# Performance work log

Hardware: AMD Instinct MI355X
Metric: run time of the kernel (lower is better)

## Reference

```python
import jax, jax.numpy as jnp
import numpy as np

NL, ND, NM = 16384, 4096, 2048   # LncRNA / Disease / MiRNA node counts
E = 262144                       # edges per relation
FEAT, HID, OUTF = 256, 64, 128
ITEMS, SIZE = 4096, 2048


def setup_inputs() -> dict:
    key = jax.random.key(0)
    ks = jax.random.split(key, 32)
    f32 = jnp.float32

    def ed(i, n_src, n_dst):
        return (jax.random.randint(ks[i], (E,), 0, n_src),
                jax.random.randint(ks[i + 1], (E,), 0, n_dst))

    src_LD, dst_LD = ed(0, NL, ND)
    src_DL, dst_DL = ed(2, ND, NL)
    src_LM, dst_LM = ed(4, NL, NM)
    src_ML, dst_ML = ed(6, NM, NL)
    src_DM, dst_DM = ed(8, ND, NM)
    src_MD, dst_MD = ed(10, NM, ND)

    inp = dict(
        h_L=jax.random.normal(ks[12], (NL, FEAT), f32),
        h_D=jax.random.normal(ks[13], (ND, FEAT), f32),
        h_M=jax.random.normal(ks[14], (NM, FEAT), f32),
        Adj=jax.random.uniform(ks[15], (SIZE, ITEMS), f32),
        src_LD=src_LD, dst_LD=dst_LD, src_DL=src_DL, dst_DL=dst_DL,
        src_LM=src_LM, dst_LM=dst_LM, src_ML=src_ML, dst_ML=dst_ML,
        src_DM=src_DM, dst_DM=dst_DM, src_MD=src_MD, dst_MD=dst_MD,
        # GraphConv weights, stacked over the 6 relations in order
        # [LvsD, DvsL, LvsM, MvsL, DvsM, MvsD]
        W1=jax.random.normal(ks[16], (6, FEAT, HID), f32) * 0.05,
        b1=jnp.zeros((6, HID), f32),
        W2=jax.random.normal(ks[17], (6, HID, HID), f32) * 0.05,
        b2=jnp.zeros((6, HID), f32),
        W3=jax.random.normal(ks[18], (6, HID, OUTF), f32) * 0.05,
        b3=jnp.zeros((6, OUTF), f32),
        # dense MLP head
        f1_w=jax.random.normal(ks[19], (ITEMS + OUTF, 256), f32) * 0.02,
        f1_b=jnp.zeros((256,), f32),
        f2_w=jax.random.normal(ks[20], (256, 512), f32) * 0.05,
        f2_b=jnp.zeros((512,), f32),
        f3_w=jax.random.normal(ks[21], (512, 1024), f32) * 0.05,
        f3_b=jnp.zeros((1024,), f32),
        f4_w=jax.random.normal(ks[22], (1024, ITEMS), f32) * 0.03,
        f4_b=jnp.zeros((ITEMS,), f32),
        size=SIZE,
        leftIndex=0,
    )
    return inp


def _gconv(x, src, dst, n_dst, W, b):
    """DGL GraphConv with norm='both': D_dst^{-1/2} A D_src^{-1/2} X W + b.
    Degrees are clamped to >=1 (DGL behavior)."""
    n_src = x.shape[0]
    ones = jnp.ones(src.shape[0], x.dtype)
    out_deg = jnp.clip(jax.ops.segment_sum(ones, src, num_segments=n_src), 1.0)
    in_deg = jnp.clip(jax.ops.segment_sum(ones, dst, num_segments=n_dst), 1.0)
    feat = x * jax.lax.rsqrt(out_deg)[:, None]
    m = jax.ops.segment_sum(feat[src], dst, num_segments=n_dst)
    m = m * jax.lax.rsqrt(in_deg)[:, None]
    return m @ W + b


def reference(h_L, h_D, h_M, Adj,
              W1, b1, W2, b2, W3, b3,
              f1_w, f1_b, f2_w, f2_b, f3_w, f3_b, f4_w, f4_b,
              src_LD, dst_LD, src_DL, dst_DL, src_LM, dst_LM,
              src_ML, dst_ML, src_DM, dst_DM, src_MD, dst_MD,
              size, leftIndex):

    def hetero_layer(hL, hD, hM, W, b):
        # aggregate='sum' over edge types per destination node type
        oD = (_gconv(hL, src_LD, dst_LD, ND, W[0], b[0])
              + _gconv(hM, src_MD, dst_MD, ND, W[5], b[5]))
        oL = (_gconv(hD, src_DL, dst_DL, NL, W[1], b[1])
              + _gconv(hM, src_ML, dst_ML, NL, W[3], b[3]))
        oM = (_gconv(hL, src_LM, dst_LM, NM, W[2], b[2])
              + _gconv(hD, src_DM, dst_DM, NM, W[4], b[4]))
        return oL, oD, oM

    hL, hD, hM = hetero_layer(h_L, h_D, h_M, W1, b1)
    hL, hD, hM = hetero_layer(hL, hD, hM, W2, b2)
    hL, hD, hM = hetero_layer(hL, hD, hM, W3, b3)

    # F.normalize(p=1, dim=1): x / max(||x||_1, 1e-12)
    l1 = jnp.maximum(jnp.sum(jnp.abs(hL), axis=1, keepdims=True), 1e-12)
    lncrna = hL / l1

    fake_embedding = lncrna[leftIndex:leftIndex + size]  # [size, OUTF]
    x = jnp.concatenate([Adj, fake_embedding], axis=1)   # [size, ITEMS+OUTF]
    x = jax.nn.relu(x @ f1_w + f1_b)
    x = jax.nn.relu(x @ f2_w + f2_b)
    x = jax.nn.relu(x @ f3_w + f3_b)
    x = jax.nn.sigmoid(x @ f4_w + f4_b)
    return (fake_embedding, x)
```

## Files before the change

### kernel.cpp

```cpp
#include <hip/hip_runtime.h>

constexpr int kNL = 16384, kND = 4096, kNM = 2048;
constexpr int kE = 262144;
constexpr int kFEAT = 256, kHID = 64, kOUTF = 128;
constexpr int kITEMS = 4096, kSIZE = 2048;
constexpr int kHB = 16;
constexpr int kZS = 128;
constexpr int kXIN = kITEMS + kOUTF;

typedef unsigned short ushort_t;
typedef unsigned int uint_t;
typedef __attribute__((ext_vector_type(8))) short short8v;
typedef __attribute__((ext_vector_type(4))) float f32x4;

struct EdgePtrs { const int* p[12]; };
struct I6 { int v[6]; };

__device__ inline ushort_t f2bf(float f) {
  unsigned u = __builtin_bit_cast(unsigned, f);
  unsigned r = u + 0x7fffu + ((u >> 16) & 1u);
  return (ushort_t)(r >> 16);
}
__device__ inline float bf2f(ushort_t b) {
  unsigned u = ((unsigned)b) << 16;
  return __builtin_bit_cast(float, u);
}
__device__ inline float bf2f_lo(uint_t v) { return __builtin_bit_cast(float, v << 16); }
__device__ inline float bf2f_hi(uint_t v) { return __builtin_bit_cast(float, v & 0xffff0000u); }

__device__ __forceinline__ void gload16(const ushort_t* g, ushort_t* l) {
  __builtin_amdgcn_global_load_lds(
      (const __attribute__((address_space(1))) void*)g,
      (__attribute__((address_space(3))) void*)l, 16, 0, 0);
}

__device__ __forceinline__ void xcd_swizzle(int& bx, int& by) {
  int gx = gridDim.x, gy = gridDim.y;
  int nwg = gx * gy;
  int orig = by * gx + bx;
  int q = nwg >> 3, r = nwg & 7;
  int xcd = orig & 7, loc = orig >> 3;
  int s = ((xcd < r) ? xcd * (q + 1) : r * (q + 1) + (xcd - r) * q) + loc;
  by = s % gy;
  bx = s / gy;
}

__global__ __launch_bounds__(256) void hist_kernel(EdgePtrs ep, uint_t* __restrict__ part) {
  __shared__ uint_t bins[16384];
  int k = blockIdx.x >> 4, chunk = blockIdx.x & (kHB - 1);
  for (int i = threadIdx.x; i < 16384; i += 256) bins[i] = 0;
  __syncthreads();
  const int* arr = ep.p[k];
  int base = chunk * (kE / kHB);
  for (int i = threadIdx.x; i < kE / kHB; i += 256)
    atomicAdd(&bins[arr[base + i]], 1u);
  __syncthreads();
  uint_t* o = part + ((size_t)blockIdx.x << 14);
  for (int i = threadIdx.x; i < 16384; i += 256) o[i] = bins[i];
}

struct PJob { const float* in; ushort_t* out; int A; int B; int C; int kind; int nblk; };
struct PJobs { PJob j[24]; int n; };

__global__ __launch_bounds__(256) void prep_kernel(PJobs jobs) {
  __shared__ float t[32][33];
  int b = blockIdx.x;
  int ji = 0;
  while (ji < jobs.n && b >= jobs.j[ji].nblk) { b -= jobs.j[ji].nblk; ++ji; }
  if (ji >= jobs.n) return;
  PJob jb = jobs.j[ji];
  if (jb.kind == 0) {
    int idx = b * 256 + threadIdx.x;
    if (idx >= jb.A) return;
    float4 v = ((const float4*)jb.in)[idx];
    ushort_t* o = jb.out + (size_t)idx * 4;
    o[0] = f2bf(v.x); o[1] = f2bf(v.y); o[2] = f2bf(v.z); o[3] = f2bf(v.w);
  } else if (jb.kind == 2) {
    int idx = b * 256 + threadIdx.x;
    if (idx >= jb.A) return;
    float4 v = ((const float4*)jb.in)[idx];
    int row = idx / jb.B, col4 = idx - row * jb.B;
    ushort_t* o = jb.out + (size_t)row * jb.C + (size_t)col4 * 4;
    o[0] = f2bf(v.x); o[1] = f2bf(v.y); o[2] = f2bf(v.z); o[3] = f2bf(v.w);
  } else {
    int K = jb.A, N = jb.B;
    int tpr = N >> 5;
    int n0 = (b % tpr) * 32, k0 = (b / tpr) * 32;
    int tx = threadIdx.x & 31, ty = threadIdx.x >> 5;
#pragma unroll
    for (int i = 0; i < 32; i += 8)
      t[ty + i][tx] = jb.in[(size_t)(k0 + ty + i) * N + n0 + tx];
    __syncthreads();
#pragma unroll
    for (int i = 0; i < 32; i += 8)
      jb.out[(size_t)(n0 + ty + i) * K + k0 + tx] = f2bf(t[tx][ty + i]);
  }
}

__global__ void reduce_finalize_kernel(const uint_t* __restrict__ part,
                                       uint_t* __restrict__ cnts,
                                       float* __restrict__ degscale) {
  int idx = blockIdx.x * 256 + threadIdx.x;
  int k = idx >> 14, bin = idx & 16383;
  uint_t s = 0;
  for (int c = 0; c < kHB; ++c) s += part[((size_t)(k * kHB + c) << 14) + bin];
  cnts[idx] = s;
  degscale[idx] = rsqrtf((float)max(s, 1u));
}

__global__ __launch_bounds__(1024) void scan_kernel(const uint_t* __restrict__ cnts,
                                                    uint_t* __restrict__ rp_all,
                                                    I6 rpoff, I6 nd) {
  __shared__ uint_t sums[1024];
  int t = blockIdx.x;
  int n = nd.v[t];
  const uint_t* c = cnts + ((size_t)(2 * t + 1) << 14);
  uint_t* rp = rp_all + rpoff.v[t];
  int tid = threadIdx.x;
  int seg = n >> 10;
  uint_t s = 0;
  for (int j = 0; j < seg; ++j) s += c[tid * seg + j];
  sums[tid] = s;
  __syncthreads();
  for (int o = 1; o < 1024; o <<= 1) {
    uint_t v = (tid >= o) ? sums[tid - o] : 0u;
    __syncthreads();
    sums[tid] += v;
    __syncthreads();
  }
  uint_t run = sums[tid] - s;
  for (int j = 0; j < seg; ++j) { rp[tid * seg + j] = run; run += c[tid * seg + j]; }
  if (tid == 1023) rp[n] = run;
}

__global__ void chunkofs_kernel(const uint_t* __restrict__ part,
                                const uint_t* __restrict__ rp_all,
                                I6 rpoff, I6 nd, uint_t* __restrict__ ofs) {
  int idx = blockIdx.x * 256 + threadIdx.x;
  int t = idx >> 14, bin = idx & 16383;
  if (bin >= nd.v[t]) return;
  uint_t run = (rp_all + rpoff.v[t])[bin];
  for (int c = 0; c < kHB; ++c) {
    ofs[((size_t)(t * kHB + c) << 14) + bin] = run;
    run += part[((size_t)((2 * t + 1) * kHB + c) << 14) + bin];
  }
}

__global__ __launch_bounds__(256) void fill_kernel(EdgePtrs ep,
                                                   const uint_t* __restrict__ ofs,
                                                   uint_t* __restrict__ csr_all) {
  __shared__ uint_t cursor[16384];
  int t = blockIdx.x >> 4, chunk = blockIdx.x & (kHB - 1);
  const uint_t* o = ofs + ((size_t)(t * kHB + chunk) << 14);
  for (int i = threadIdx.x; i < 16384; i += 256) cursor[i] = o[i];
  __syncthreads();
  const int* srcp = ep.p[2 * t];
  const int* dstp = ep.p[2 * t + 1];
  int base = chunk * (kE / kHB);
  uint_t* csr = csr_all + (size_t)t * kE;
  for (int i = threadIdx.x; i < kE / kHB; i += 256) {
    int e = base + i;
    int d = dstp[e];
    uint_t pos = atomicAdd(&cursor[d], 1u);
    csr[pos] = (uint_t)srcp[e];
  }
}

__global__ __launch_bounds__(256) void gemm_bf16_kernel(
    const ushort_t* __restrict__ A, const ushort_t* __restrict__ Bt,
    const float* __restrict__ Cin, void* __restrict__ out, int outBf16,
    int M, int N, int K, int ldb,
    const float* __restrict__ bias, int act,
    int kChunk, float* __restrict__ partOut) {
  __shared__ ushort_t As[2][8192];
  __shared__ ushort_t Bs[2][8192];
  int tid = threadIdx.x;
  int wave = tid >> 6, lane = tid & 63;
  int bx = blockIdx.x, by = blockIdx.y;
  xcd_swizzle(bx, by);
  int brow = by * 128, bcol = bx * 128;
  int kStart = partOut ? blockIdx.z * kChunk : 0;
  int kLen = partOut ? kChunk : K;
  int nsteps = kLen >> 6;

  int rowBase = tid >> 3;
  int u = (tid & 7) ^ (rowBase & 7);
  const ushort_t* gA = A + (size_t)(brow + rowBase) * K + kStart + u * 8;
  const ushort_t* gB = Bt + (size_t)(bcol + rowBase) * ldb + kStart + u * 8;

  int fr = lane & 15, fq = lane >> 4;
  f32x4 acc[2][8] = {};

#define STAGE_G(buf, koff)                                              \
  do {                                                                  \
    _Pragma("unroll")                                                   \
    for (int j = 0; j < 4; ++j) {                                       \
      gload16(gA + (size_t)j * 32 * K + (koff), &As[buf][j * 2048 + tid * 8]);   \
      gload16(gB + (size_t)j * 32 * ldb + (koff), &Bs[buf][j * 2048 + tid * 8]); \
    }                                                                   \
  } while (0)

  STAGE_G(0, 0);
  int cur = 0;
  for (int i = 0; i < nsteps; ++i) {
    __syncthreads();
    if (i + 1 < nsteps) STAGE_G(cur ^ 1, (i + 1) * 64);
#pragma unroll
    for (int kk = 0; kk < 2; ++kk) {
      short8v af[2], bfr[8];
#pragma unroll
      for (int mi = 0; mi < 2; ++mi) {
        int row = wave * 32 + mi * 16 + fr;
        af[mi] = *(const short8v*)(&As[cur][row * 64 + (((kk * 4 + fq) ^ (row & 7)) * 8)]);
      }
#pragma unroll
      for (int ni = 0; ni < 8; ++ni) {
        int row = ni * 16 + fr;
        bfr[ni] = *(const short8v*)(&Bs[cur][row * 64 + (((kk * 4 + fq) ^ (row & 7)) * 8)]);
      }
#pragma unroll
      for (int mi = 0; mi < 2; ++mi)
#pragma unroll
        for (int ni = 0; ni < 8; ++ni)
          acc[mi][ni] = __builtin_amdgcn_mfma_f32_16x16x32_bf16(af[mi], bfr[ni], acc[mi][ni], 0, 0, 0);
    }
    cur ^= 1;
  }
#undef STAGE_G

  if (partOut) {
    float* o = partOut + (size_t)blockIdx.z * M * N;
#pragma unroll
    for (int mi = 0; mi < 2; ++mi)
#pragma unroll
      for (int ni = 0; ni < 8; ++ni)
#pragma unroll
        for (int r = 0; r < 4; ++r) {
          int row = brow + wave * 32 + mi * 16 + fq * 4 + r;
          int col = bcol + ni * 16 + fr;
          o[(size_t)row * N + col] = acc[mi][ni][r];
        }
    return;
  }
#pragma unroll
  for (int mi = 0; mi < 2; ++mi)
#pragma unroll
    for (int ni = 0; ni < 8; ++ni)
#pragma unroll
      for (int r = 0; r < 4; ++r) {
        int row = brow + wave * 32 + mi * 16 + fq * 4 + r;
        int col = bcol + ni * 16 + fr;
        float v = acc[mi][ni][r];
        if (Cin) v += Cin[(size_t)row * N + col];
        if (bias) v += bias[col];
        if (act == 1) v = fmaxf(v, 0.0f);
        else if (act == 2) v = 1.0f / (1.0f + expf(-v));
        if (outBf16) ((ushort_t*)out)[(size_t)row * N + col] = f2bf(v);
        else ((float*)out)[(size_t)row * N + col] = v;
      }
}

__global__ __launch_bounds__(512) void gemm256_kernel(
    const ushort_t* __restrict__ A, const ushort_t* __restrict__ Bt,
    float* __restrict__ out, int M, int N, int K,
    const float* __restrict__ bias) {
  __shared__ ushort_t As[3][16384];
  __shared__ ushort_t Bs[3][8192];
  int tid = threadIdx.x;
  int wave = tid >> 6, lane = tid & 63;
  int bx = blockIdx.x, by = blockIdx.y;
  xcd_swizzle(bx, by);
  int fr = lane & 15, fq = lane >> 4;
  int wm = wave >> 2, wn = wave & 3;

  int rquot = tid >> 3;
  int uslot = (tid & 7) ^ (rquot & 7);
  const ushort_t* gA = A + (size_t)(by * 256 + rquot) * K + uslot * 8;
  const ushort_t* gB = Bt + (size_t)(bx * 128 + rquot) * K + uslot * 8;

  f32x4 acc[8][2] = {};
  int nsteps = K >> 6;

#define SG_A(b_, t_, j_) gload16(gA + (size_t)(j_) * 64 * K + (size_t)(t_) * 64, &As[b_][(j_) * 4096 + tid * 8])
#define SG_B(b_, t_, j_) gload16(gB + (size_t)(j_) * 64 * K + (size_t)(t_) * 64, &Bs[b_][(j_) * 4096 + tid * 8])

  SG_A(0, 0, 0); SG_A(0, 0, 1); SG_A(0, 0, 2); SG_A(0, 0, 3); SG_B(0, 0, 0); SG_B(0, 0, 1);
  SG_A(1, 1, 0); SG_A(1, 1, 1); SG_A(1, 1, 2); SG_A(1, 1, 3); SG_B(1, 1, 0); SG_B(1, 1, 1);
  asm volatile("s_waitcnt vmcnt(6)" ::: "memory");
  __builtin_amdgcn_s_barrier();

  short8v bf[2][2];

#define PHASE(p_)                                                            \
  {                                                                          \
    short8v af[4][2];                                                        \
    _Pragma("unroll")                                                        \
    for (int q = 0; q < 4; ++q) {                                            \
      int row = wm * 128 + (4 * (p_) + q) * 16 + fr;                         \
      int base = row * 64;                                                   \
      af[q][0] = *(const short8v*)(&As[b][base + ((fq ^ (row & 7)) * 8)]);   \
      af[q][1] = *(const short8v*)(&As[b][base + (((4 + fq) ^ (row & 7)) * 8)]); \
    }                                                                        \
    if ((p_) == 0) {                                                         \
      _Pragma("unroll")                                                      \
      for (int q = 0; q < 2; ++q) {                                          \
        int row = wn * 32 + q * 16 + fr;                                     \
        int base = row * 64;                                                 \
        bf[q][0] = *(const short8v*)(&Bs[b][base + ((fq ^ (row & 7)) * 8)]); \
        bf[q][1] = *(const short8v*)(&Bs[b][base + (((4 + fq) ^ (row & 7)) * 8)]); \
      }                                                                      \
      if (doStage) { SG_A(sb, t + 2, 0); SG_A(sb, t + 2, 1); SG_A(sb, t + 2, 2); SG_A(sb, t + 2, 3); } \
    } else {                                                                 \
      if (doStage) { SG_B(sb, t + 2, 0); SG_B(sb, t + 2, 1); }               \
      if (t + 2 < nsteps)      asm volatile("s_waitcnt vmcnt(6)" ::: "memory"); \
      else if (t + 1 < nsteps) asm volatile("s_waitcnt vmcnt(0)" ::: "memory"); \
    }                                                                        \
    __builtin_amdgcn_s_barrier();                                            \
    asm volatile("s_waitcnt lgkmcnt(0)" ::: "memory");                       \
    __builtin_amdgcn_s_setprio(1);                                           \
    _Pragma("unroll")                                                        \
    for (int kk = 0; kk < 2; ++kk)                                           \
      _Pragma("unroll")                                                      \
      for (int q = 0; q < 4; ++q)                                            \
        _Pragma("unroll")                                                    \
        for (int ni = 0; ni < 2; ++ni)                                       \
          acc[4 * (p_) + q][ni] = __builtin_amdgcn_mfma_f32_16x16x32_bf16(af[q][kk], bf[ni][kk], acc[4 * (p_) + q][ni], 0, 0, 0); \
    __builtin_amdgcn_s_setprio(0);                                           \
    __builtin_amdgcn_s_barrier();                                            \
  }

  for (int t = 0; t < nsteps; ++t) {
    int b = t % 3, sb = (t + 2) % 3;
    bool doStage = (t + 2 < nsteps);
    PHASE(0);
    PHASE(1);
  }
#undef PHASE
#undef SG_A
#undef SG_B

#pragma unroll
  for (int mi = 0; mi < 8; ++mi)
#pragma unroll
    for (int ni = 0; ni < 2; ++ni)
#pragma unroll
      for (int r = 0; r < 4; ++r) {
        int row = by * 256 + wm * 128 + mi * 16 + fq * 4 + r;
        int col = bx * 128 + wn * 32 + ni * 16 + fr;
        float v = acc[mi][ni][r] + bias[col];
        out[(size_t)row * N + col] = 1.0f / (1.0f + expf(-v));
      }
}

struct ZDesc { const ushort_t* A; const ushort_t* Bt; ushort_t* out;
               const float* rs0; const float* rs1; int M; int K; };
struct ZDescs { ZDesc d[3]; };

__global__ __launch_bounds__(256) void zgemm_batched_kernel(ZDescs ds) {
  __shared__ ushort_t As[2][8192];
  __shared__ ushort_t Bs[2][8192];
  ZDesc de = ds.d[blockIdx.z];
  int gy = gridDim.y;
  int yq = gy >> 3;
  int ys = (blockIdx.y & 7) * yq + (blockIdx.y >> 3);
  int brow = ys * 128;
  if (brow >= de.M) return;
  int K = de.K;
  int nsteps = K >> 6;
  if (nsteps == 0) nsteps = 1;
  int kkMax = (K >= 64) ? 2 : 1;
  int tid = threadIdx.x;
  int wave = tid >> 6, lane = tid & 63;

  int rowBase = tid >> 3;
  int u = (tid & 7) ^ (rowBase & 7);
  const ushort_t* gA = de.A + (size_t)(brow + rowBase) * K + u * 8;
  const ushort_t* gB = de.Bt + (size_t)rowBase * K + u * 8;

  int fr = lane & 15, fq = lane >> 4;
  f32x4 acc[2][8] = {};

#define STAGE_Z(buf, koff)                                              \
  do {                                                                  \
    _Pragma("unroll")                                                   \
    for (int j = 0; j < 4; ++j) {                                       \
      gload16(gA + (size_t)j * 32 * K + (koff), &As[buf][j * 2048 + tid * 8]); \
      gload16(gB + (size_t)j * 32 * K + (koff), &Bs[buf][j * 2048 + tid * 8]); \
    }                                                                   \
  } while (0)

  STAGE_Z(0, 0);
  int cur = 0;
  for (int i = 0; i < nsteps; ++i) {
    __syncthreads();
    if (i + 1 < nsteps) STAGE_Z(cur ^ 1, (i + 1) * 64);
#pragma unroll
    for (int kk = 0; kk < 2; ++kk) {
      if (kk >= kkMax) break;
      short8v af[2], bfr[8];
#pragma unroll
      for (int mi = 0; mi < 2; ++mi) {
        int row = wave * 32 + mi * 16 + fr;
        af[mi] = *(const short8v*)(&As[cur][row * 64 + (((kk * 4 + fq) ^ (row & 7)) * 8)]);
      }
#pragma unroll
      for (int ni = 0; ni < 8; ++ni) {
        int row = ni * 16 + fr;
        bfr[ni] = *(const short8v*)(&Bs[cur][row * 64 + (((kk * 4 + fq) ^ (row & 7)) * 8)]);
      }
#pragma unroll
      for (int mi = 0; mi < 2; ++mi)
#pragma unroll
        for (int ni = 0; ni < 8; ++ni)
          acc[mi][ni] = __builtin_amdgcn_mfma_f32_16x16x32_bf16(af[mi], bfr[ni], acc[mi][ni], 0, 0, 0);
    }
    cur ^= 1;
  }
#undef STAGE_Z

#pragma unroll
  for (int mi = 0; mi < 2; ++mi)
#pragma unroll
    for (int ni = 0; ni < 8; ++ni) {
      const float* rs = (ni < 4) ? de.rs0 : de.rs1;
#pragma unroll
      for (int r = 0; r < 4; ++r) {
        int row = brow + wave * 32 + mi * 16 + fq * 4 + r;
        int col = ni * 16 + fr;
        de.out[(size_t)row * 128 + col] = f2bf(acc[mi][ni][r] * rs[row]);
      }
    }
}

struct GDesc { const ushort_t* z0; const uint_t* rp0; const uint_t* cs0; const float* s0;
               const ushort_t* z1; const uint_t* rp1; const uint_t* cs1; const float* s1;
               const float* b0; const float* b1; ushort_t* out; int nd; };
struct GDescs { GDesc d[3]; };

__device__ __forceinline__ void gpair(const ushort_t* __restrict__ z,
                                      const uint_t* __restrict__ cs,
                                      uint_t e, uint_t ee, int h, int cp,
                                      float& ax, float& ay) {
  float x0 = 0, y0 = 0, x1 = 0, y1 = 0, x2 = 0, y2 = 0, x3 = 0, y3 = 0;
  for (; e + 8 <= ee; e += 8) {
    uint_t s0 = cs[e + 0 + h], s1 = cs[e + 2 + h], s2 = cs[e + 4 + h], s3 = cs[e + 6 + h];
    uint_t v0 = *(const uint_t*)(z + (size_t)s0 * kZS + 2 * cp);
    uint_t v1 = *(const uint_t*)(z + (size_t)s1 * kZS + 2 * cp);
    uint_t v2 = *(const uint_t*)(z + (size_t)s2 * kZS + 2 * cp);
    uint_t v3 = *(const uint_t*)(z + (size_t)s3 * kZS + 2 * cp);
    x0 += bf2f_lo(v0); y0 += bf2f_hi(v0);
    x1 += bf2f_lo(v1); y1 += bf2f_hi(v1);
    x2 += bf2f_lo(v2); y2 += bf2f_hi(v2);
    x3 += bf2f_lo(v3); y3 += bf2f_hi(v3);
  }
  for (; e + 2 <= ee; e += 2) {
    uint_t v = *(const uint_t*)(z + (size_t)cs[e + h] * kZS + 2 * cp);
    x0 += bf2f_lo(v); y0 += bf2f_hi(v);
  }
  if (h == 0 && e < ee) {
    uint_t v = *(const uint_t*)(z + (size_t)cs[e] * kZS + 2 * cp);
    x0 += bf2f_lo(v); y0 += bf2f_hi(v);
  }
  ax = (x0 + x1) + (x2 + x3);
  ay = (y0 + y1) + (y2 + y3);
}

__global__ __launch_bounds__(256) void gather_batched_kernel(GDescs ds) {
  GDesc de = ds.d[blockIdx.z];
  int d = blockIdx.x * 4 + (threadIdx.x >> 6);
  if (d >= de.nd) return;
  int lane = threadIdx.x & 63;
  int h = lane >> 5, cp = lane & 31;
  float ax0, ay0, ax1, ay1;
  gpair(de.z0, de.cs0, de.rp0[d], de.rp0[d + 1], h, cp, ax0, ay0);
  gpair(de.z1, de.cs1, de.rp1[d], de.rp1[d + 1], h, cp, ax1, ay1);
  float s0 = de.s0[d], s1 = de.s1[d];
  float vx = ax0 * s0 + ax1 * s1;
  float vy = ay0 * s0 + ay1 * s1;
  vx += __shfl_xor(vx, 32);
  vy += __shfl_xor(vy, 32);
  if (h == 0) {
    int c0 = 2 * cp;
    vx += de.b0[c0] + de.b1[c0];
    vy += de.b0[c0 + 1] + de.b1[c0 + 1];
    uint_t pack = (uint_t)f2bf(vx) | ((uint_t)f2bf(vy) << 16);
    *(uint_t*)(de.out + (size_t)d * 64 + c0) = pack;
  }
}

__device__ __forceinline__ void gone128(const ushort_t* __restrict__ z,
                                        const uint_t* __restrict__ cs,
                                        uint_t e, uint_t ee, int l,
                                        float& ax, float& ay) {
  float x0 = 0, y0 = 0, x1 = 0, y1 = 0, x2 = 0, y2 = 0, x3 = 0, y3 = 0;
  for (; e + 4 <= ee; e += 4) {
    uint_t s0 = cs[e], s1 = cs[e + 1], s2 = cs[e + 2], s3 = cs[e + 3];
    uint_t v0 = *(const uint_t*)(z + (size_t)s0 * 128 + 2 * l);
    uint_t v1 = *(const uint_t*)(z + (size_t)s1 * 128 + 2 * l);
    uint_t v2 = *(const uint_t*)(z + (size_t)s2 * 128 + 2 * l);
    uint_t v3 = *(const uint_t*)(z + (size_t)s3 * 128 + 2 * l);
    x0 += bf2f_lo(v0); y0 += bf2f_hi(v0);
    x1 += bf2f_lo(v1); y1 += bf2f_hi(v1);
    x2 += bf2f_lo(v2); y2 += bf2f_hi(v2);
    x3 += bf2f_lo(v3); y3 += bf2f_hi(v3);
  }
  for (; e < ee; ++e) {
    uint_t v = *(const uint_t*)(z + (size_t)cs[e] * 128 + 2 * l);
    x0 += bf2f_lo(v); y0 += bf2f_hi(v);
  }
  ax = (x0 + x1) + (x2 + x3);
  ay = (y0 + y1) + (y2 + y3);
}

__global__ __launch_bounds__(256) void gather128_l1_kernel(
    const ushort_t* __restrict__ zD, const uint_t* __restrict__ rpD, const uint_t* __restrict__ csD,
    const float* __restrict__ sInD,
    const ushort_t* __restrict__ zM, const uint_t* __restrict__ rpM, const uint_t* __restrict__ csM,
    const float* __restrict__ sInM,
    const float* __restrict__ bD, const float* __restrict__ bM,
    float* __restrict__ emb, ushort_t* __restrict__ embb, int embStride) {
  int d = blockIdx.x * 4 + (threadIdx.x >> 6);
  int l = threadIdx.x & 63;
  float axD, ayD, axM, ayM;
  gone128(zD, csD, rpD[d], rpD[d + 1], l, axD, ayD);
  gone128(zM, csM, rpM[d], rpM[d + 1], l, axM, ayM);
  float sD = sInD[d], sM = sInM[d];
  int c0 = 2 * l;
  float v0 = axD * sD + axM * sM + bD[c0] + bM[c0];
  float v1 = ayD * sD + ayM * sM + bD[c0 + 1] + bM[c0 + 1];
  float a = fabsf(v0) + fabsf(v1);
#pragma unroll
  for (int o = 32; o > 0; o >>= 1) a += __shfl_xor(a, o);
  float l1 = fmaxf(a, 1e-12f);
  float e0 = v0 / l1, e1 = v1 / l1;
  float2 fe = {e0, e1};
  *(float2*)(emb + (size_t)d * kOUTF + c0) = fe;
  uint_t pack = (uint_t)f2bf(e0) | ((uint_t)f2bf(e1) << 16);
  *(uint_t*)(embb + (size_t)d * embStride + c0) = pack;
}

__global__ void reducek_kernel(const float* __restrict__ P, void* __restrict__ out,
                               int outBf16, int n4, int S, int N,
                               const float* __restrict__ bias, int act) {
  int idx = blockIdx.x * 256 + threadIdx.x;
  if (idx >= n4) return;
  float4 a = ((const float4*)P)[idx];
  for (int s = 1; s < S; ++s) {
    float4 b = ((const float4*)P)[(size_t)s * n4 + idx];
    a.x += b.x; a.y += b.y; a.z += b.z; a.w += b.w;
  }
  float v[4] = {a.x, a.y, a.z, a.w};
  int c0 = (idx * 4) % N;
#pragma unroll
  for (int j = 0; j < 4; ++j) {
    if (bias) v[j] += bias[c0 + j];
    if (act == 1) v[j] = fmaxf(v[j], 0.0f);
    else if (act == 2) v[j] = 1.0f / (1.0f + expf(-v[j]));
  }
  if (outBf16) {
    ushort_t* o = (ushort_t*)out + (size_t)idx * 4;
    o[0] = f2bf(v[0]); o[1] = f2bf(v[1]); o[2] = f2bf(v[2]); o[3] = f2bf(v[3]);
  } else {
    float4 r = {v[0], v[1], v[2], v[3]};
    ((float4*)out)[idx] = r;
  }
}

extern "C" void kernel_launch(void* const* d_in, const int* in_sizes, int n_in,
                              void* d_out, int out_size, void* d_ws, size_t ws_size,
                              hipStream_t stream) {
  const float* h_L = (const float*)d_in[0];
  const float* h_D = (const float*)d_in[1];
  const float* h_M = (const float*)d_in[2];
  const float* Adj = (const float*)d_in[3];
  EdgePtrs ep;
  for (int i = 0; i < 12; ++i) ep.p[i] = (const int*)d_in[4 + i];
  const float* W[3]  = {(const float*)d_in[16], (const float*)d_in[18], (const float*)d_in[20]};
  const float* Bb[3] = {(const float*)d_in[17], (const float*)d_in[19], (const float*)d_in[21]};
  const float* f1_w = (const float*)d_in[22];
  const float* f1_b = (const float*)d_in[23];
  const float* f2_w = (const float*)d_in[24];
  const float* f2_b = (const float*)d_in[25];
  const float* f3_w = (const float*)d_in[26];
  const float* f3_b = (const float*)d_in[27];
  const float* f4_w = (const float*)d_in[28];
  const float* f4_b = (const float*)d_in[29];

  float* ws = (float*)d_ws;
  size_t off = 0;
  auto allocF = [&](size_t n) { float* p = ws + off; off += (n + 3) & ~(size_t)3; return p; };
  auto allocU = [&](size_t n) { return (uint_t*)allocF(n); };
  auto allocB = [&](size_t n) { return (ushort_t*)allocF((n + 1) / 2); };

  uint_t* part   = allocU((size_t)12 * kHB * 16384);
  uint_t* cnts   = allocU((size_t)12 * 16384);
  float*  degscale = allocF((size_t)12 * 16384);
  uint_t* rp_all = allocU(45062 + 2);
  uint_t* ofs    = allocU((size_t)6 * kHB * 16384);
  uint_t* csr    = allocU((size_t)6 * kE);
  ushort_t* hLb  = allocB((size_t)kNL * kFEAT);
  ushort_t* hDb  = allocB((size_t)kND * kFEAT);
  ushort_t* hMb  = allocB((size_t)kNM * kFEAT);
  ushort_t* xin  = allocB((size_t)kSIZE * kXIN);
  ushort_t* aLb  = allocB((size_t)kNL * kHID);
  ushort_t* aDb  = allocB((size_t)kND * kHID);
  ushort_t* aMb  = allocB((size_t)kNM * kHID);
  ushort_t* WLt  = allocB((size_t)128 * kFEAT);
  ushort_t* WDt  = allocB((size_t)128 * kFEAT);
  ushort_t* WMt  = allocB((size_t)128 * kFEAT);
  ushort_t* WL2t = allocB((size_t)128 * kHID);
  ushort_t* WD2t = allocB((size_t)128 * kHID);
  ushort_t* WM2t = allocB((size_t)128 * kHID);
  ushort_t* W3t1 = allocB((size_t)kOUTF * kHID);
  ushort_t* W3t3 = allocB((size_t)kOUTF * kHID);
  ushort_t* f1t  = allocB((size_t)256 * kXIN);
  ushort_t* f2t  = allocB((size_t)512 * 256);
  ushort_t* f3t  = allocB((size_t)1024 * 512);
  ushort_t* f4t  = allocB((size_t)kITEMS * 1024);
  ushort_t* x1b  = allocB((size_t)kSIZE * 256);
  ushort_t* x2b  = allocB((size_t)kSIZE * 512);
  ushort_t* x3b  = allocB((size_t)kSIZE * 1024);

  int S1 = 1, S2 = 1, S3 = 1;
  float* partK = nullptr;
  size_t avail = (ws_size / 4 > off) ? ws_size / 4 - off - 64 : 0;
  if (avail >= (size_t)4 * kSIZE * 512 + 16) {
    partK = allocF((size_t)4 * kSIZE * 512);
    S1 = 6; S2 = 4; S3 = 2;
  }

  ushort_t* zL  = (ushort_t*)part;
  ushort_t* zD  = zL + (size_t)kNL * kZS;
  ushort_t* zM  = zD + (size_t)kND * kZS;
  ushort_t* zD3 = zM + (size_t)kNM * kZS;
  ushort_t* zM3 = zD3 + (size_t)kND * kZS;

  I6 ndI; const int ndst_[6] = {kND, kNL, kNM, kNL, kNM, kND};
  for (int t = 0; t < 6; ++t) ndI.v[t] = ndst_[t];
  I6 rpo; { int r = 0; for (int t = 0; t < 6; ++t) { rpo.v[t] = r; r += ndst_[t] + 1; } }
  auto dsc = [&](int k) { return degscale + ((size_t)k << 14); };

  hist_kernel<<<12 * kHB, 256, 0, stream>>>(ep, part);

  PJobs pj; int nj = 0; int totblk = 0;
  auto addCvt = [&](const float* in, ushort_t* out, size_t n) {
    int n4 = (int)(n / 4);
    pj.j[nj] = {in, out, n4, 0, 0, 0, (n4 + 255) / 256}; totblk += pj.j[nj].nblk; ++nj;
  };
  auto addStrided = [&](const float* in, ushort_t* out, size_t n, int rowLen, int stride) {
    int n4 = (int)(n / 4);
    pj.j[nj] = {in, out, n4, rowLen / 4, stride, 2, (n4 + 255) / 256}; totblk += pj.j[nj].nblk; ++nj;
  };
  auto addT = [&](const float* in, ushort_t* out, int K, int N) {
    pj.j[nj] = {in, out, K, N, 0, 1, (N / 32) * (K / 32)}; totblk += pj.j[nj].nblk; ++nj;
  };
  addCvt(h_L, hLb, (size_t)kNL * kFEAT);
  addCvt(h_D, hDb, (size_t)kND * kFEAT);
  addCvt(h_M, hMb, (size_t)kNM * kFEAT);
  addStrided(Adj, xin, (size_t)kSIZE * kITEMS, kITEMS, kXIN);
  addT(W[0] + (size_t)0 * kFEAT * kHID, WLt + (size_t)0 * kFEAT, kFEAT, kHID);
  addT(W[0] + (size_t)2 * kFEAT * kHID, WLt + (size_t)64 * kFEAT, kFEAT, kHID);
  addT(W[0] + (size_t)1 * kFEAT * kHID, WDt + (size_t)0 * kFEAT, kFEAT, kHID);
  addT(W[0] + (size_t)4 * kFEAT * kHID, WDt + (size_t)64 * kFEAT, kFEAT, kHID);
  addT(W[0] + (size_t)3 * kFEAT * kHID, WMt + (size_t)0 * kFEAT, kFEAT, kHID);
  addT(W[0] + (size_t)5 * kFEAT * kHID, WMt + (size_t)64 * kFEAT, kFEAT, kHID);
  addT(W[1] + (size_t)0 * kHID * kHID, WL2t + (size_t)0 * kHID, kHID, kHID);
  addT(W[1] + (size_t)2 * kHID * kHID, WL2t + (size_t)64 * kHID, kHID, kHID);
  addT(W[1] + (size_t)1 * kHID * kHID, WD2t + (size_t)0 * kHID, kHID, kHID);
  addT(W[1] + (size_t)4 * kHID * kHID, WD2t + (size_t)64 * kHID, kHID, kHID);
  addT(W[1] + (size_t)3 * kHID * kHID, WM2t + (size_t)0 * kHID, kHID, kHID);
  addT(W[1] + (size_t)5 * kHID * kHID, WM2t + (size_t)64 * kHID, kHID, kHID);
  addT(W[2] + (size_t)1 * kHID * kOUTF, W3t1, kHID, kOUTF);
  addT(W[2] + (size_t)3 * kHID * kOUTF, W3t3, kHID, kOUTF);
  addT(f1_w, f1t, kXIN, 256);
  addT(f2_w, f2t, 256, 512);
  addT(f3_w, f3t, 512, 1024);
  addT(f4_w, f4t, 1024, kITEMS);
  pj.n = nj;
  prep_kernel<<<totblk, 256, 0, stream>>>(pj);

  reduce_finalize_kernel<<<12 * 16384 / 256, 256, 0, stream>>>(part, cnts, degscale);
  scan_kernel<<<6, 1024, 0, stream>>>(cnts, rp_all, rpo, ndI);
  chunkofs_kernel<<<6 * 16384 / 256, 256, 0, stream>>>(part, rp_all, rpo, ndI, ofs);
  fill_kernel<<<6 * kHB, 256, 0, stream>>>(ep, ofs, csr);

  const ushort_t* curb[3] = {hLb, hDb, hMb};
  for (int layer = 0; layer < 2; ++layer) {
    int K = (layer == 0) ? kFEAT : kHID;
    const ushort_t* WtL = (layer == 0) ? WLt : WL2t;
    const ushort_t* WtD = (layer == 0) ? WDt : WD2t;
    const ushort_t* WtM = (layer == 0) ? WMt : WM2t;
    const float* bl = Bb[layer];
    ZDescs zd;
    zd.d[0] = {curb[0], WtL, zL, dsc(0), dsc(4),  kNL, K};
    zd.d[1] = {curb[1], WtD, zD, dsc(2), dsc(8),  kND, K};
    zd.d[2] = {curb[2], WtM, zM, dsc(6), dsc(10), kNM, K};
    zgemm_batched_kernel<<<dim3(1, kNL / 128, 3), 256, 0, stream>>>(zd);
    if (layer == 0) {
      GDescs gd;
      gd.d[0] = {zD, rp_all + rpo.v[1], csr + (size_t)1 * kE, dsc(3),
                 zM, rp_all + rpo.v[3], csr + (size_t)3 * kE, dsc(7),
                 bl + 1 * kHID, bl + 3 * kHID, aLb, kNL};
      gd.d[1] = {zL, rp_all + rpo.v[0], csr + (size_t)0 * kE, dsc(1),
                 zM + 64, rp_all + rpo.v[5], csr + (size_t)5 * kE, dsc(11),
                 bl + 0 * kHID, bl + 5 * kHID, aDb, kND};
      gd.d[2] = {zL + 64, rp_all + rpo.v[2], csr + (size_t)2 * kE, dsc(5),
                 zD + 64, rp_all + rpo.v[4], csr + (size_t)4 * kE, dsc(9),
                 bl + 2 * kHID, bl + 4 * kHID, aMb, kNM};
      gather_batched_kernel<<<dim3(kNL / 4, 1, 3), 256, 0, stream>>>(gd);
    } else {
      GDescs gd;
      gd.d[0] = {zL, rp_all + rpo.v[0], csr + (size_t)0 * kE, dsc(1),
                 zM + 64, rp_all + rpo.v[5], csr + (size_t)5 * kE, dsc(11),
                 bl + 0 * kHID, bl + 5 * kHID, aDb, kND};
      gd.d[1] = {zL + 64, rp_all + rpo.v[2], csr + (size_t)2 * kE, dsc(5),
                 zD + 64, rp_all + rpo.v[4], csr + (size_t)4 * kE, dsc(9),
                 bl + 2 * kHID, bl + 4 * kHID, aMb, kNM};
      gd.d[2] = gd.d[1];
      gather_batched_kernel<<<dim3(kND / 4, 1, 2), 256, 0, stream>>>(gd);
    }
    curb[0] = aLb; curb[1] = aDb; curb[2] = aMb;
  }

  float* emb  = (float*)d_out;
  float* outx = (float*)d_out + (size_t)kSIZE * kOUTF;
  {
    ZDescs zd;
    zd.d[0] = {curb[1], W3t1, zD3, dsc(2), dsc(2), kND, kHID};
    zd.d[1] = {curb[2], W3t3, zM3, dsc(6), dsc(6), kNM, kHID};
    zd.d[2] = zd.d[1];
    zgemm_batched_kernel<<<dim3(1, kND / 128, 2), 256, 0, stream>>>(zd);
    gather128_l1_kernel<<<kSIZE / 4, 256, 0, stream>>>(
        zD3, rp_all + rpo.v[1], csr + (size_t)1 * kE, dsc(3),
        zM3, rp_all + rpo.v[3], csr + (size_t)3 * kE, dsc(7),
        Bb[2] + 1 * kOUTF, Bb[2] + 3 * kOUTF, emb, xin + kITEMS, kXIN);
  }

  if (S1 > 1) {
    gemm_bf16_kernel<<<dim3(2, 16, S1), 256, 0, stream>>>(
        xin, f1t, nullptr, nullptr, 0, kSIZE, 256, kXIN, kXIN,
        nullptr, 0, kXIN / S1, partK);
    int n4 = kSIZE * 256 / 4;
    reducek_kernel<<<(n4 + 255) / 256, 256, 0, stream>>>(
        partK, x1b, 1, n4, S1, 256, f1_b, 1);
  } else {
    gemm_bf16_kernel<<<dim3(2, 16, 1), 256, 0, stream>>>(
        xin, f1t, nullptr, x1b, 1, kSIZE, 256, kXIN, kXIN, f1_b, 1, 0, nullptr);
  }
  if (S2 > 1) {
    gemm_bf16_kernel<<<dim3(4, 16, S2), 256, 0, stream>>>(
        x1b, f2t, nullptr, nullptr, 0, kSIZE, 512, 256, 256,
        nullptr, 0, 256 / S2, partK);
    int n4 = kSIZE * 512 / 4;
    reducek_kernel<<<(n4 + 255) / 256, 256, 0, stream>>>(
        partK, x2b, 1, n4, S2, 512, f2_b, 1);
  } else {
    gemm_bf16_kernel<<<dim3(4, 16, 1), 256, 0, stream>>>(
        x1b, f2t, nullptr, x2b, 1, kSIZE, 512, 256, 256, f2_b, 1, 0, nullptr);
  }
  if (S3 > 1) {
    gemm_bf16_kernel<<<dim3(8, 16, S3), 256, 0, stream>>>(
        x2b, f3t, nullptr, nullptr, 0, kSIZE, 1024, 512, 512,
        nullptr, 0, 512 / S3, partK);
    int n4 = kSIZE * 1024 / 4;
    reducek_kernel<<<(n4 + 255) / 256, 256, 0, stream>>>(
        partK, x3b, 1, n4, S3, 1024, f3_b, 1);
  } else {
    gemm_bf16_kernel<<<dim3(8, 16, 1), 256, 0, stream>>>(
        x2b, f3t, nullptr, x3b, 1, kSIZE, 1024, 512, 512, f3_b, 1, 0, nullptr);
  }
  gemm256_kernel<<<dim3(kITEMS / 128, kSIZE / 256), 512, 0, stream>>>(
      x3b, f4t, outx, kSIZE, kITEMS, 1024, f4_b);
}
```

Baseline: 311.7 us.

## Replace LDS double-buffered z-GEMM with per-wave direct-load MFMA tiles and skip unused columns

The batched feature-times-weight GEMM no longer stages A and B tiles through double-buffered shared memory. Each wave now loads its MFMA fragments straight from global memory and computes a 64x64 output tile, with two column blocks per 256-row block. A per-descriptor column range (nlo/nhi) lets layer 2 skip the D and M output columns whose results are never consumed. This drops the LDS traffic and barriers and removes redundant work, but loses shared-memory reuse, so each A and B fragment is reread from global or L2 by several waves.

```diff
diff --git a/kernel.cpp b/kernel.cpp
--- a/kernel.cpp
+++ b/kernel.cpp
@@ -353,83 +353,52 @@
 }
 
 struct ZDesc { const ushort_t* A; const ushort_t* Bt; ushort_t* out;
-               const float* rs0; const float* rs1; int M; int K; };
+               const float* rs0; const float* rs1; int M; int K; int nlo; int nhi; };
 struct ZDescs { ZDesc d[3]; };
 
 __global__ __launch_bounds__(256) void zgemm_batched_kernel(ZDescs ds) {
-  __shared__ ushort_t As[2][8192];
-  __shared__ ushort_t Bs[2][8192];
   ZDesc de = ds.d[blockIdx.z];
-  int gy = gridDim.y;
-  int yq = gy >> 3;
-  int ys = (blockIdx.y & 7) * yq + (blockIdx.y >> 3);
-  int brow = ys * 128;
-  if (brow >= de.M) return;
+  int wave = threadIdx.x >> 6, lane = threadIdx.x & 63;
+  int wrow = blockIdx.y * 256 + wave * 64;
+  if (wrow >= de.M) return;
+  int wcol = blockIdx.x * 64;
+  int ni0 = wcol >> 4;
+  if (ni0 < de.nlo * 1 || ni0 + 4 > de.nhi) {
+    if (ni0 < de.nlo || ni0 >= de.nhi) return;
+  }
   int K = de.K;
-  int nsteps = K >> 6;
-  if (nsteps == 0) nsteps = 1;
-  int kkMax = (K >= 64) ? 2 : 1;
-  int tid = threadIdx.x;
-  int wave = tid >> 6, lane = tid & 63;
-
-  int rowBase = tid >> 3;
-  int u = (tid & 7) ^ (rowBase & 7);
-  const ushort_t* gA = de.A + (size_t)(brow + rowBase) * K + u * 8;
-  const ushort_t* gB = de.Bt + (size_t)rowBase * K + u * 8;
-
   int fr = lane & 15, fq = lane >> 4;
-  f32x4 acc[2][8] = {};
-
-#define STAGE_Z(buf, koff)                                              \
-  do {                                                                  \
-    _Pragma("unroll")                                                   \
-    for (int j = 0; j < 4; ++j) {                                       \
-      gload16(gA + (size_t)j * 32 * K + (koff), &As[buf][j * 2048 + tid * 8]); \
-      gload16(gB + (size_t)j * 32 * K + (koff), &Bs[buf][j * 2048 + tid * 8]); \
-    }                                                                   \
-  } while (0)
-
-  STAGE_Z(0, 0);
-  int cur = 0;
-  for (int i = 0; i < nsteps; ++i) {
-    __syncthreads();
-    if (i + 1 < nsteps) STAGE_Z(cur ^ 1, (i + 1) * 64);
-#pragma unroll
-    for (int kk = 0; kk < 2; ++kk) {
-      if (kk >= kkMax) break;
-      short8v af[2], bfr[8];
-#pragma unroll
-      for (int mi = 0; mi < 2; ++mi) {
-        int row = wave * 32 + mi * 16 + fr;
-        af[mi] = *(const short8v*)(&As[cur][row * 64 + (((kk * 4 + fq) ^ (row & 7)) * 8)]);
-      }
-#pragma unroll
-      for (int ni = 0; ni < 8; ++ni) {
-        int row = ni * 16 + fr;
-        bfr[ni] = *(const short8v*)(&Bs[cur][row * 64 + (((kk * 4 + fq) ^ (row & 7)) * 8)]);
-      }
-#pragma unroll
-      for (int mi = 0; mi < 2; ++mi)
-#pragma unroll
-        for (int ni = 0; ni < 8; ++ni)
-          acc[mi][ni] = __builtin_amdgcn_mfma_f32_16x16x32_bf16(af[mi], bfr[ni], acc[mi][ni], 0, 0, 0);
+
+  const ushort_t* pA = de.A + (size_t)(wrow + fr) * K + fq * 8;
+  const ushort_t* pB = de.Bt + (size_t)(wcol + fr) * K + fq * 8;
+
+  f32x4 acc[4][4] = {};
+#pragma unroll 2
+  for (int k0 = 0; k0 < K; k0 += 32) {
+    short8v af[4], bf[4];
+#pragma unroll
+    for (int i = 0; i < 4; ++i) {
+      af[i] = *(const short8v*)(pA + (size_t)i * 16 * K + k0);
+      bf[i] = *(const short8v*)(pB + (size_t)i * 16 * K + k0);
     }
-    cur ^= 1;
-  }
-#undef STAGE_Z
-
-#pragma unroll
-  for (int mi = 0; mi < 2; ++mi)
-#pragma unroll
-    for (int ni = 0; ni < 8; ++ni) {
-      const float* rs = (ni < 4) ? de.rs0 : de.rs1;
+#pragma unroll
+    for (int mi = 0; mi < 4; ++mi)
+#pragma unroll
+      for (int ni = 0; ni < 4; ++ni)
+        acc[mi][ni] = __builtin_amdgcn_mfma_f32_16x16x32_bf16(af[mi], bf[ni], acc[mi][ni], 0, 0, 0);
+  }
+
+  const float* rs = (wcol == 0) ? de.rs0 : de.rs1;
+#pragma unroll
+  for (int mi = 0; mi < 4; ++mi)
+#pragma unroll
+    for (int ni = 0; ni < 4; ++ni)
 #pragma unroll
       for (int r = 0; r < 4; ++r) {
-        int row = brow + wave * 32 + mi * 16 + fq * 4 + r;
-        int col = ni * 16 + fr;
+        int row = wrow + mi * 16 + fq * 4 + r;
+        int col = wcol + ni * 16 + fr;
         de.out[(size_t)row * 128 + col] = f2bf(acc[mi][ni][r] * rs[row]);
       }
-    }
 }
 
 struct GDesc { const ushort_t* z0; const uint_t* rp0; const uint_t* cs0; const float* s0;
@@ -692,10 +661,16 @@
     const ushort_t* WtM = (layer == 0) ? WMt : WM2t;
     const float* bl = Bb[layer];
     ZDescs zd;
-    zd.d[0] = {curb[0], WtL, zL, dsc(0), dsc(4),  kNL, K};
-    zd.d[1] = {curb[1], WtD, zD, dsc(2), dsc(8),  kND, K};
-    zd.d[2] = {curb[2], WtM, zM, dsc(6), dsc(10), kNM, K};
-    zgemm_batched_kernel<<<dim3(1, kNL / 128, 3), 256, 0, stream>>>(zd);
+    if (layer == 0) {
+      zd.d[0] = {curb[0], WtL, zL, dsc(0), dsc(4),  kNL, K, 0, 8};
+      zd.d[1] = {curb[1], WtD, zD, dsc(2), dsc(8),  kND, K, 0, 8};
+      zd.d[2] = {curb[2], WtM, zM, dsc(6), dsc(10), kNM, K, 0, 8};
+    } else {
+      zd.d[0] = {curb[0], WtL, zL, dsc(0), dsc(4),  kNL, K, 0, 8};
+      zd.d[1] = {curb[1], WtD, zD, dsc(2), dsc(8),  kND, K, 4, 8};
+      zd.d[2] = {curb[2], WtM, zM, dsc(6), dsc(10), kNM, K, 4, 8};
+    }
+    zgemm_batched_kernel<<<dim3(2, kNL / 256, 3), 256, 0, stream>>>(zd);
     if (layer == 0) {
       GDescs gd;
       gd.d[0] = {zD, rp_all + rpo.v[1], csr + (size_t)1 * kE, dsc(3),
@@ -726,10 +701,10 @@
   float* outx = (float*)d_out + (size_t)kSIZE * kOUTF;
   {
     ZDescs zd;
-    zd.d[0] = {curb[1], W3t1, zD3, dsc(2), dsc(2), kND, kHID};
-    zd.d[1] = {curb[2], W3t3, zM3, dsc(6), dsc(6), kNM, kHID};
+    zd.d[0] = {curb[1], W3t1, zD3, dsc(2), dsc(2), kND, kHID, 0, 8};
+    zd.d[1] = {curb[2], W3t3, zM3, dsc(6), dsc(6), kNM, kHID, 0, 8};
     zd.d[2] = zd.d[1];
-    zgemm_batched_kernel<<<dim3(1, kND / 128, 2), 256, 0, stream>>>(zd);
+    zgemm_batched_kernel<<<dim3(2, kND / 256, 2), 256, 0, stream>>>(zd);
     gather128_l1_kernel<<<kSIZE / 4, 256, 0, stream>>>(
         zD3, rp_all + rpo.v[1], csr + (size_t)1 * kE, dsc(3),
         zM3, rp_all + rpo.v[3], csr + (size_t)3 * kE, dsc(7),
```

Measured after the change: 322.6 us. 3.5% more time.
